# Optimization experiments

Hardware: AMD Instinct MI355X
Metric: run time of the kernel (lower is better)

The kernel has to match this reference:

```python
import jax, jax.numpy as jnp
import numpy as np

B, S, E, H = 4, 2048, 1024, 16
D = E // H  # head dim = 64


def setup_inputs() -> dict:
    key = jax.random.key(0)
    ks = jax.random.split(key, 8)
    scale = 0.02
    return {
        "query": jax.random.normal(ks[0], (B, S, E), jnp.float32),
        "keys": jax.random.normal(ks[1], (B, S, E), jnp.float32),
        "values": jax.random.normal(ks[2], (B, S, E), jnp.float32),
        "mask": jnp.ones((B, 1, 1, S), jnp.int32),
        "Wq": jax.random.normal(ks[3], (D, D), jnp.float32) * scale,
        "Wk": jax.random.normal(ks[4], (D, D), jnp.float32) * scale,
        "Wv": jax.random.normal(ks[5], (D, D), jnp.float32) * scale,
        "Wf": jax.random.normal(ks[6], (E, E), jnp.float32) * scale,
        "bf": jax.random.normal(ks[7], (E,), jnp.float32) * scale,
    }


def reference(query, keys, values, mask, Wq, Wk, Wv, Wf, bf):
    b, sq, _ = query.shape
    sk = keys.shape[1]
    # reshape to heads: [b, s, H, D]
    q = query.reshape(b, sq, H, D)
    k = keys.reshape(b, sk, H, D)
    v = values.reshape(b, sk, H, D)
    # per-head linear projections (torch Linear: x @ W.T, no bias)
    q = jnp.einsum('bshd,ed->bshe', q, Wq)
    k = jnp.einsum('bshd,ed->bshe', k, Wk)
    v = jnp.einsum('bshd,ed->bshe', v, Wv)
    # scores [b, h, q, k]
    scores = jnp.einsum('bqhd,bkhd->bhqk', q, k)
    scores = jnp.where(mask == 0, -jnp.inf, scores)
    attn = jax.nn.softmax(scores / jnp.sqrt(jnp.float32(D)), axis=3)
    # context [b, q, h, d] -> [b, q, E]
    ctx = jnp.einsum('bhqk,bkhd->bqhd', attn, v).reshape(b, sq, E)
    return ctx @ Wf.T + bf
```

## Files before the change

kernel.cpp:

```cpp
#include <hip/hip_runtime.h>

#define B_ 4
#define S_ 2048
#define E_ 1024
#define H_ 16
#define D_ 64

typedef unsigned short u16;
typedef unsigned int u32;
typedef __bf16 bf16x8 __attribute__((ext_vector_type(8)));
typedef float f32x4 __attribute__((ext_vector_type(4)));
typedef u16 u16x8 __attribute__((ext_vector_type(8)));
typedef u16 u16x4 __attribute__((ext_vector_type(4)));

#if defined(__has_builtin)
#if __has_builtin(__builtin_amdgcn_exp2f)
#define EXP2F(x) __builtin_amdgcn_exp2f(x)
#else
#define EXP2F(x) exp2f(x)
#endif
#else
#define EXP2F(x) exp2f(x)
#endif

__device__ __forceinline__ u16 bfbits(float f) {
  __bf16 h = (__bf16)f;
  return __builtin_bit_cast(u16, h);
}
__device__ __forceinline__ f32x4 mfma16(bf16x8 a, bf16x8 b, f32x4 c) {
  return __builtin_amdgcn_mfma_f32_16x16x32_bf16(a, b, c, 0, 0, 0);
}
__device__ __forceinline__ bf16x8 lds_ld8(const u16* base, int off) {
  return *reinterpret_cast<const bf16x8*>(reinterpret_cast<const char*>(base) + off);
}
__device__ __forceinline__ void gload_lds16(const u16* g, u16* l) {
  __builtin_amdgcn_global_load_lds((const __attribute__((address_space(1))) void*)g,
                                   (__attribute__((address_space(3))) void*)l, 16, 0, 0);
}

__global__ __launch_bounds__(256) void proj_kernel(
    const float* __restrict__ qin, const float* __restrict__ kin, const float* __restrict__ vin,
    const float* __restrict__ Wq, const float* __restrict__ Wk, const float* __restrict__ Wv,
    const float* __restrict__ Wf,
    u16* __restrict__ qo, u16* __restrict__ ko, u16* __restrict__ vo, u16* __restrict__ wfo)
{
  const int t = threadIdx.x;
  const int tensor = blockIdx.z >> 2, b = blockIdx.z & 3;

  if (tensor == 3) {
    int chunk = ((blockIdx.z & 3) * 16 + blockIdx.y) * 16 + blockIdx.x;
    int i = chunk * 256 + t;
    float4 f = reinterpret_cast<const float4*>(Wf)[i];
    u16x4 h4;
    h4[0] = bfbits(f.x); h4[1] = bfbits(f.y); h4[2] = bfbits(f.z); h4[3] = bfbits(f.w);
    reinterpret_cast<u16x4*>(wfo)[i] = h4;
    return;
  }

  __shared__ __align__(16) u16 Al[128 * 64];
  __shared__ __align__(16) u16 Wl[64 * 64];
  const int w = t >> 6, l = t & 63, lg = l >> 4, ln = l & 15;
  const int h = blockIdx.y, s0 = blockIdx.x * 128;

  const float* x; const float* W; float scale;
  if (tensor == 0)      { x = qin; W = Wq; scale = 0.125f * 1.44269504f; }
  else if (tensor == 1) { x = kin; W = Wk; scale = 1.0f; }
  else                  { x = vin; W = Wv; scale = 1.0f; }

  {
    const int e = t >> 2, d0 = (t & 3) * 16;
    const float4* wr = reinterpret_cast<const float4*>(W + e * 64 + d0);
    float4 f0 = wr[0], f1 = wr[1], f2 = wr[2], f3 = wr[3];
    u16x8 p0, p1;
    p0[0]=bfbits(f0.x*scale); p0[1]=bfbits(f0.y*scale); p0[2]=bfbits(f0.z*scale); p0[3]=bfbits(f0.w*scale);
    p0[4]=bfbits(f1.x*scale); p0[5]=bfbits(f1.y*scale); p0[6]=bfbits(f1.z*scale); p0[7]=bfbits(f1.w*scale);
    p1[0]=bfbits(f2.x*scale); p1[1]=bfbits(f2.y*scale); p1[2]=bfbits(f2.z*scale); p1[3]=bfbits(f2.w*scale);
    p1[4]=bfbits(f3.x*scale); p1[5]=bfbits(f3.y*scale); p1[6]=bfbits(f3.z*scale); p1[7]=bfbits(f3.w*scale);
    *reinterpret_cast<u16x8*>(reinterpret_cast<char*>(Wl) + ((e*128 + d0*2     ) ^ ((e & 7) << 4))) = p0;
    *reinterpret_cast<u16x8*>(reinterpret_cast<char*>(Wl) + ((e*128 + d0*2 + 16) ^ ((e & 7) << 4))) = p1;
  }
  {
    const int row = t >> 1, d0 = (t & 1) * 32;
    const float4* xr = reinterpret_cast<const float4*>(x + ((size_t)(b * S_ + s0 + row)) * E_ + h * D_ + d0);
    #pragma unroll
    for (int c = 0; c < 4; ++c) {
      float4 f0 = xr[2 * c], f1 = xr[2 * c + 1];
      u16x8 pk;
      pk[0]=bfbits(f0.x); pk[1]=bfbits(f0.y); pk[2]=bfbits(f0.z); pk[3]=bfbits(f0.w);
      pk[4]=bfbits(f1.x); pk[5]=bfbits(f1.y); pk[6]=bfbits(f1.z); pk[7]=bfbits(f1.w);
      *reinterpret_cast<u16x8*>(reinterpret_cast<char*>(Al) +
          ((row * 128 + (d0 + 8 * c) * 2) ^ ((row & 7) << 4))) = pk;
    }
  }
  __syncthreads();

  bf16x8 wb[4][2];
  #pragma unroll
  for (int nn = 0; nn < 4; ++nn) {
    int brow = nn * 16 + ln;
    int bo = (brow * 128 + lg * 16) ^ ((ln & 7) << 4);
    wb[nn][0] = lds_ld8(Wl, bo);
    wb[nn][1] = lds_ld8(Wl, bo ^ 64);
  }
  f32x4 acc[2][4] = {};
  #pragma unroll
  for (int sub = 0; sub < 2; ++sub) {
    int arow = 32 * w + 16 * sub + ln;
    int ao = (arow * 128 + lg * 16) ^ ((ln & 7) << 4);
    bf16x8 a0 = lds_ld8(Al, ao), a1 = lds_ld8(Al, ao ^ 64);
    #pragma unroll
    for (int nn = 0; nn < 4; ++nn) {
      acc[sub][nn] = mfma16(a0, wb[nn][0], acc[sub][nn]);
      acc[sub][nn] = mfma16(a1, wb[nn][1], acc[sub][nn]);
    }
  }

  if (tensor < 2) {
    u16* o = (tensor == 0) ? qo : ko;
    const size_t hb = ((size_t)(b * H_ + h)) * (S_ * D_);
    #pragma unroll
    for (int sub = 0; sub < 2; ++sub)
      #pragma unroll
      for (int nn = 0; nn < 4; ++nn)
        #pragma unroll
        for (int r = 0; r < 4; ++r)
          o[hb + (size_t)(s0 + 32*w + 16*sub + 4*lg + r) * D_ + nn*16 + ln] = bfbits(acc[sub][nn][r]);
  } else {
    const size_t hb = ((size_t)(b * H_ + h)) * (D_ * S_);
    #pragma unroll
    for (int sub = 0; sub < 2; ++sub)
      #pragma unroll
      for (int nn = 0; nn < 4; ++nn)
        #pragma unroll
        for (int r = 0; r < 4; ++r) {
          int scol = s0 + 32*w + 16*sub + 4*lg + r;
          int sl = scol & 63;
          int c = (sl & 3) | (((sl >> 4) & 1) << 2) | (((sl >> 2) & 3) << 3) | ((sl >> 5) << 5);
          vo[hb + (size_t)(nn*16 + ln) * S_ + (scol & ~63) + c] = bfbits(acc[sub][nn][r]);
        }
  }
}

#define QK_PHASE(SCW)                                                          \
  {                                                                            \
    __builtin_amdgcn_s_setprio(1);                                             \
    _Pragma("unroll")                                                          \
    for (int kn = 0; kn < 4; ++kn) {                                           \
      int o0 = ((ln * 128 + lg * 16) ^ ((ln & 7) << 4)) + kn * 2048;           \
      bf16x8 ka0 = lds_ld8(Kc, o0), ka1 = lds_ld8(Kc, o0 ^ 64);                \
      _Pragma("unroll")                                                        \
      for (int sub = 0; sub < 2; ++sub) {                                      \
        f32x4 z = {0.f, 0.f, 0.f, 0.f};                                        \
        z = mfma16(ka0, qb[sub][0], z);                                        \
        z = mfma16(ka1, qb[sub][1], z);                                        \
        SCW[sub][kn] = z;                                                      \
      }                                                                        \
    }                                                                          \
    __builtin_amdgcn_s_setprio(0);                                             \
  }

#define EXPPV_PHASE(SCR, KV0PREV)                                              \
  {                                                                            \
    if (!allone) {                                                             \
      const int kv0p = (KV0PREV);                                              \
      _Pragma("unroll")                                                        \
      for (int kn = 0; kn < 4; ++kn) {                                         \
        const int4 m4 = *reinterpret_cast<const int4*>(                        \
            mask + b * S_ + kv0p + kn * 16 + lg * 4);                          \
        const int* mp = reinterpret_cast<const int*>(&m4);                     \
        _Pragma("unroll")                                                      \
        for (int r = 0; r < 4; ++r)                                            \
          if (mp[r] == 0) { SCR[0][kn][r] = -1e30f; SCR[1][kn][r] = -1e30f; }  \
      }                                                                        \
    }                                                                          \
    bf16x8 pa[2][2];                                                           \
    _Pragma("unroll")                                                          \
    for (int sub = 0; sub < 2; ++sub)                                          \
      _Pragma("unroll")                                                        \
      for (int kn = 0; kn < 4; ++kn)                                           \
        _Pragma("unroll")                                                      \
        for (int r = 0; r < 4; ++r)                                            \
          pa[sub][kn >> 1][(kn & 1) * 4 + r] = (__bf16)EXP2F(SCR[sub][kn][r]); \
    __builtin_amdgcn_s_setprio(1);                                             \
    _Pragma("unroll")                                                          \
    for (int sub = 0; sub < 2; ++sub) {                                        \
      lacc[sub] = mfma16(pa[sub][0], ones, lacc[sub]);                         \
      lacc[sub] = mfma16(pa[sub][1], ones, lacc[sub]);                         \
    }                                                                          \
    _Pragma("unroll")                                                          \
    for (int kh = 0; kh < 2; ++kh)                                             \
      _Pragma("unroll")                                                        \
      for (int dn = 0; dn < 4; ++dn)                                           \
        _Pragma("unroll")                                                      \
        for (int sub = 0; sub < 2; ++sub)                                      \
          oacc[sub][dn] = mfma16(pa[sub][kh], vf[kh][dn], oacc[sub][dn]);      \
    __builtin_amdgcn_s_setprio(0);                                             \
  }

#define VREAD_PHASE                                                            \
  _Pragma("unroll")                                                            \
  for (int kh = 0; kh < 2; ++kh)                                               \
    _Pragma("unroll")                                                          \
    for (int dn = 0; dn < 4; ++dn) {                                           \
      int vo0 = ((ln * 128 + 16 * lg + 64 * kh) ^ ((ln & 7) << 4)) + dn * 2048;\
      vf[kh][dn] = lds_ld8(Vc, vo0);                                           \
    }

#define ATTN_ITER(KT, SCW, SCR, CUR, LAST)                                     \
  {                                                                            \
    const u16* Kc = &Kl[CUR][0];                                               \
    const u16* Vc = &Vl[CUR][0];                                               \
    if (!(LAST)) {                                                             \
      const int nk = ((KT) + 1) * 64;                                          \
      gload_lds16(kg + nk * D_, kd + ((CUR) ^ 1) * 4096);                      \
      gload_lds16(vg + nk,      vd + ((CUR) ^ 1) * 4096);                      \
    }                                                                          \
    QK_PHASE(SCW)                                                              \
    EXPPV_PHASE(SCR, ((KT) - 1) * 64)                                          \
    VREAD_PHASE                                                                \
    if (!(LAST)) {                                                             \
      asm volatile("s_waitcnt vmcnt(0)" ::: "memory");                         \
      __syncthreads();                                                         \
    }                                                                          \
  }

__global__ __launch_bounds__(512, 2) void attn_kernel(
    const u16* __restrict__ qw,
    const u16* __restrict__ kw,
    const u16* __restrict__ vtw,
    const int* __restrict__ mask,
    u16* __restrict__ ctx)
{
  __shared__ __align__(16) u16 Kl[2][64 * 64];
  __shared__ __align__(16) u16 Vl[2][64 * 64];
  __shared__ int s_allone;

  const int t = threadIdx.x, w = t >> 6, l = t & 63, lg = l >> 4, ln = l & 15;
  const int hb = blockIdx.x;
  const int b = hb >> 4;
  const int q0 = blockIdx.y * 256;
  const size_t koff = (size_t)hb * (S_ * D_);
  const size_t voff = (size_t)hb * (D_ * S_);

  if (t == 0) s_allone = 1;
  __syncthreads();

  const int srow = t >> 3, scol = (t & 7) ^ ((t >> 3) & 7);
  const u16* kg = kw + koff + srow * D_ + scol * 8;
  const u16* vg = vtw + voff + (size_t)srow * S_ + scol * 8;
  u16* kd = &Kl[0][0] + t * 8;
  u16* vd = &Vl[0][0] + t * 8;

  gload_lds16(kg, kd);
  gload_lds16(vg, vd);

  {
    const int4 m4 = *reinterpret_cast<const int4*>(mask + b * S_ + t * 4);
    if (!(m4.x && m4.y && m4.z && m4.w)) s_allone = 0;
  }

  bf16x8 qb[2][2];
  #pragma unroll
  for (int sub = 0; sub < 2; ++sub) {
    const u16* qp = qw + koff + (size_t)(q0 + 32*w + 16*sub + ln) * D_ + 8*lg;
    qb[sub][0] = *reinterpret_cast<const bf16x8*>(qp);
    qb[sub][1] = *reinterpret_cast<const bf16x8*>(qp + 32);
  }

  u16x8 ob;
  #pragma unroll
  for (int i = 0; i < 8; ++i) ob[i] = 0x3F80;
  const bf16x8 ones = __builtin_bit_cast(bf16x8, ob);

  f32x4 oacc[2][4] = {};
  f32x4 lacc[2] = {};
  f32x4 scA[2][4], scB[2][4];
  bf16x8 vf[2][4];

  asm volatile("s_waitcnt vmcnt(0)" ::: "memory");
  __syncthreads();
  const int allone = s_allone;

  {
    const u16* Kc = &Kl[0][0];
    const u16* Vc = &Vl[0][0];
    gload_lds16(kg + 64 * D_, kd + 4096);
    gload_lds16(vg + 64,      vd + 4096);
    QK_PHASE(scA)
    VREAD_PHASE
    asm volatile("s_waitcnt vmcnt(0)" ::: "memory");
    __syncthreads();
  }

  for (int kt = 1; kt < 31; kt += 2) {
    ATTN_ITER(kt,     scB, scA, 1, false)
    ATTN_ITER(kt + 1, scA, scB, 0, false)
  }
  ATTN_ITER(31, scB, scA, 1, true)
  EXPPV_PHASE(scB, 31 * 64)

  #pragma unroll
  for (int sub = 0; sub < 2; ++sub) {
    #pragma unroll
    for (int r = 0; r < 4; ++r) {
      float linv = 1.f / lacc[sub][r];
      int qrow = q0 + 32 * w + 16 * sub + 4 * lg + r;
      size_t base = ((size_t)b * S_ + qrow) * E_ + (hb & 15) * D_;
      #pragma unroll
      for (int dn = 0; dn < 4; ++dn)
        ctx[base + dn * 16 + ln] = bfbits(oacc[sub][dn][r] * linv);
    }
  }
}

__global__ __launch_bounds__(256, 2) void outproj_kernel(
    const u16* __restrict__ ctx, const u16* __restrict__ wf,
    const float* __restrict__ bias, float* __restrict__ out)
{
  __shared__ __align__(16) u16 Al[2][128 * 64];
  __shared__ __align__(16) u16 Bl[2][128 * 64];
  const int t = threadIdx.x, w = t >> 6, l = t & 63, lg = l >> 4, ln = l & 15;
  const int wm = w >> 1, wn = w & 1;
  const int m0 = blockIdx.x * 128, n0 = blockIdx.y * 128;
  f32x4 acc[4][4] = {};

  const u16* ag[4]; const u16* bg[4]; int ldo[4];
  #pragma unroll
  for (int it = 0; it < 4; ++it) {
    int j = it * 256 + t, row = j >> 3, c = (j & 7) ^ (row & 7);
    ag[it] = ctx + (size_t)(m0 + row) * E_ + c * 8;
    bg[it] = wf  + (size_t)(n0 + row) * E_ + c * 8;
    ldo[it] = j * 8;
  }
  #pragma unroll
  for (int it = 0; it < 4; ++it) {
    gload_lds16(ag[it], &Al[0][0] + ldo[it]);
    gload_lds16(bg[it], &Bl[0][0] + ldo[it]);
  }
  asm volatile("s_waitcnt vmcnt(0)" ::: "memory");
  __syncthreads();

  int cur = 0;
  for (int kt = 0; kt < E_ / 64; ++kt) {
    if (kt + 1 < E_ / 64) {
      const int k0 = (kt + 1) * 64;
      #pragma unroll
      for (int it = 0; it < 4; ++it) {
        gload_lds16(ag[it] + k0, &Al[cur ^ 1][0] + ldo[it]);
        gload_lds16(bg[it] + k0, &Bl[cur ^ 1][0] + ldo[it]);
      }
    }
    const u16* Ac = &Al[cur][0]; const u16* Bc = &Bl[cur][0];

    bf16x8 af[4][2], bff[4][2];
    #pragma unroll
    for (int ms = 0; ms < 4; ++ms) {
      int ar = 64 * wm + 16 * ms + ln;
      int ao = (ar * 128 + lg * 16) ^ ((ln & 7) << 4);
      af[ms][0] = lds_ld8(Ac, ao); af[ms][1] = lds_ld8(Ac, ao ^ 64);
    }
    #pragma unroll
    for (int ns = 0; ns < 4; ++ns) {
      int br = 64 * wn + 16 * ns + ln;
      int bo = (br * 128 + lg * 16) ^ ((ln & 7) << 4);
      bff[ns][0] = lds_ld8(Bc, bo); bff[ns][1] = lds_ld8(Bc, bo ^ 64);
    }
    __builtin_amdgcn_s_setprio(1);
    #pragma unroll
    for (int ms = 0; ms < 4; ++ms)
      #pragma unroll
      for (int ns = 0; ns < 4; ++ns) {
        acc[ms][ns] = mfma16(af[ms][0], bff[ns][0], acc[ms][ns]);
        acc[ms][ns] = mfma16(af[ms][1], bff[ns][1], acc[ms][ns]);
      }
    __builtin_amdgcn_s_setprio(0);

    if (kt + 1 < E_ / 64) {
      asm volatile("s_waitcnt vmcnt(0)" ::: "memory");
      __syncthreads();
      cur ^= 1;
    }
  }

  #pragma unroll
  for (int ns = 0; ns < 4; ++ns) {
    float bv = bias[n0 + 64 * wn + 16 * ns + ln];
    #pragma unroll
    for (int ms = 0; ms < 4; ++ms)
      #pragma unroll
      for (int r = 0; r < 4; ++r)
        out[(size_t)(m0 + 64*wm + 16*ms + 4*lg + r) * E_ + n0 + 64*wn + 16*ns + ln] =
            acc[ms][ns][r] + bv;
  }
}

extern "C" void kernel_launch(void* const* d_in, const int* in_sizes, int n_in,
                              void* d_out, int out_size, void* d_ws, size_t ws_size,
                              hipStream_t stream)
{
  const float* q   = (const float*)d_in[0];
  const float* k   = (const float*)d_in[1];
  const float* v   = (const float*)d_in[2];
  const int*  mask = (const int*) d_in[3];
  const float* Wq  = (const float*)d_in[4];
  const float* Wk  = (const float*)d_in[5];
  const float* Wv  = (const float*)d_in[6];
  const float* Wf  = (const float*)d_in[7];
  const float* bfv = (const float*)d_in[8];
  float* out = (float*)d_out;

  const size_t NQKV = (size_t)B_ * H_ * S_ * D_;
  const size_t NCTX = (size_t)B_ * S_ * E_;
  u16* q_ws   = (u16*)d_ws;
  u16* k_ws   = q_ws + NQKV;
  u16* v_ws   = k_ws + NQKV;
  u16* ctx_ws = v_ws + NQKV;
  u16* wf_ws  = ctx_ws + NCTX;

  proj_kernel<<<dim3(S_ / 128, H_, 16), dim3(256), 0, stream>>>(
      q, k, v, Wq, Wk, Wv, Wf, q_ws, k_ws, v_ws, wf_ws);
  attn_kernel<<<dim3(B_ * H_, S_ / 256), dim3(512), 0, stream>>>(
      q_ws, k_ws, v_ws, mask, ctx_ws);
  outproj_kernel<<<dim3((B_ * S_) / 128, E_ / 128), dim3(256), 0, stream>>>(
      ctx_ws, wf_ws, bfv, out);
}
```

Before: 127.9 us.

## Replace software-pipelined QK/PV schedule with 4-buffer two-tile-per-sync attention loop

Removes the cross-iteration software pipeline, in which the QK scores of tile k were computed alongside the exp and PV of tile k-1 and V fragments were preloaded into registers. Each tile is now computed in one pass, with V read from LDS right where it is used. LDS staging grows from two to four K/V buffers so two tiles are loaded per barrier, halving the number of syncs. Launch bounds change to request 4 blocks per CU, which raises register pressure. The loss of QK/softmax overlap and the doubled LDS footprint may hurt latency hiding and occupancy.

```diff
diff --git a/kernel.cpp b/kernel.cpp
--- a/kernel.cpp
+++ b/kernel.cpp
@@ -141,8 +141,11 @@
   }
 }
 
-#define QK_PHASE(SCW)                                                          \
+#define COMPUTE_TILE(KT, BUF)                                                  \
   {                                                                            \
+    const u16* Kc = &Kl[BUF][0];                                               \
+    const u16* Vc = &Vl[BUF][0];                                               \
+    f32x4 sc[2][4];                                                            \
     __builtin_amdgcn_s_setprio(1);                                             \
     _Pragma("unroll")                                                          \
     for (int kn = 0; kn < 4; ++kn) {                                           \
@@ -153,24 +156,20 @@
         f32x4 z = {0.f, 0.f, 0.f, 0.f};                                        \
         z = mfma16(ka0, qb[sub][0], z);                                        \
         z = mfma16(ka1, qb[sub][1], z);                                        \
-        SCW[sub][kn] = z;                                                      \
+        sc[sub][kn] = z;                                                       \
       }                                                                        \
     }                                                                          \
     __builtin_amdgcn_s_setprio(0);                                             \
-  }
-
-#define EXPPV_PHASE(SCR, KV0PREV)                                              \
-  {                                                                            \
     if (!allone) {                                                             \
-      const int kv0p = (KV0PREV);                                              \
+      const int kv0 = (KT) * 64;                                               \
       _Pragma("unroll")                                                        \
       for (int kn = 0; kn < 4; ++kn) {                                         \
         const int4 m4 = *reinterpret_cast<const int4*>(                        \
-            mask + b * S_ + kv0p + kn * 16 + lg * 4);                          \
+            mask + b * S_ + kv0 + kn * 16 + lg * 4);                           \
         const int* mp = reinterpret_cast<const int*>(&m4);                     \
         _Pragma("unroll")                                                      \
         for (int r = 0; r < 4; ++r)                                            \
-          if (mp[r] == 0) { SCR[0][kn][r] = -1e30f; SCR[1][kn][r] = -1e30f; }  \
+          if (mp[r] == 0) { sc[0][kn][r] = -1e30f; sc[1][kn][r] = -1e30f; }    \
       }                                                                        \
     }                                                                          \
     bf16x8 pa[2][2];                                                           \
@@ -180,7 +179,7 @@
       for (int kn = 0; kn < 4; ++kn)                                           \
         _Pragma("unroll")                                                      \
         for (int r = 0; r < 4; ++r)                                            \
-          pa[sub][kn >> 1][(kn & 1) * 4 + r] = (__bf16)EXP2F(SCR[sub][kn][r]); \
+          pa[sub][kn >> 1][(kn & 1) * 4 + r] = (__bf16)EXP2F(sc[sub][kn][r]);  \
     __builtin_amdgcn_s_setprio(1);                                             \
     _Pragma("unroll")                                                          \
     for (int sub = 0; sub < 2; ++sub) {                                        \
@@ -190,49 +189,25 @@
     _Pragma("unroll")                                                          \
     for (int kh = 0; kh < 2; ++kh)                                             \
       _Pragma("unroll")                                                        \
-      for (int dn = 0; dn < 4; ++dn)                                           \
+      for (int dn = 0; dn < 4; ++dn) {                                         \
+        int vo0 = ((ln * 128 + 16 * lg + 64 * kh) ^ ((ln & 7) << 4)) + dn * 2048; \
+        bf16x8 vb = lds_ld8(Vc, vo0);                                          \
         _Pragma("unroll")                                                      \
         for (int sub = 0; sub < 2; ++sub)                                      \
-          oacc[sub][dn] = mfma16(pa[sub][kh], vf[kh][dn], oacc[sub][dn]);      \
+          oacc[sub][dn] = mfma16(pa[sub][kh], vb, oacc[sub][dn]);              \
+      }                                                                        \
     __builtin_amdgcn_s_setprio(0);                                             \
   }
 
-#define VREAD_PHASE                                                            \
-  _Pragma("unroll")                                                            \
-  for (int kh = 0; kh < 2; ++kh)                                               \
-    _Pragma("unroll")                                                          \
-    for (int dn = 0; dn < 4; ++dn) {                                           \
-      int vo0 = ((ln * 128 + 16 * lg + 64 * kh) ^ ((ln & 7) << 4)) + dn * 2048;\
-      vf[kh][dn] = lds_ld8(Vc, vo0);                                           \
-    }
-
-#define ATTN_ITER(KT, SCW, SCR, CUR, LAST)                                     \
-  {                                                                            \
-    const u16* Kc = &Kl[CUR][0];                                               \
-    const u16* Vc = &Vl[CUR][0];                                               \
-    if (!(LAST)) {                                                             \
-      const int nk = ((KT) + 1) * 64;                                          \
-      gload_lds16(kg + nk * D_, kd + ((CUR) ^ 1) * 4096);                      \
-      gload_lds16(vg + nk,      vd + ((CUR) ^ 1) * 4096);                      \
-    }                                                                          \
-    QK_PHASE(SCW)                                                              \
-    EXPPV_PHASE(SCR, ((KT) - 1) * 64)                                          \
-    VREAD_PHASE                                                                \
-    if (!(LAST)) {                                                             \
-      asm volatile("s_waitcnt vmcnt(0)" ::: "memory");                         \
-      __syncthreads();                                                         \
-    }                                                                          \
-  }
-
-__global__ __launch_bounds__(512, 2) void attn_kernel(
+__global__ __launch_bounds__(512, 4) void attn_kernel(
     const u16* __restrict__ qw,
     const u16* __restrict__ kw,
     const u16* __restrict__ vtw,
     const int* __restrict__ mask,
     u16* __restrict__ ctx)
 {
-  __shared__ __align__(16) u16 Kl[2][64 * 64];
-  __shared__ __align__(16) u16 Vl[2][64 * 64];
+  __shared__ __align__(16) u16 Kl[4][64 * 64];
+  __shared__ __align__(16) u16 Vl[4][64 * 64];
   __shared__ int s_allone;
 
   const int t = threadIdx.x, w = t >> 6, l = t & 63, lg = l >> 4, ln = l & 15;
@@ -248,11 +223,14 @@
   const int srow = t >> 3, scol = (t & 7) ^ ((t >> 3) & 7);
   const u16* kg = kw + koff + srow * D_ + scol * 8;
   const u16* vg = vtw + voff + (size_t)srow * S_ + scol * 8;
-  u16* kd = &Kl[0][0] + t * 8;
-  u16* vd = &Vl[0][0] + t * 8;
-
-  gload_lds16(kg, kd);
-  gload_lds16(vg, vd);
+  u16* kd[4]; u16* vd[4];
+  #pragma unroll
+  for (int i = 0; i < 4; ++i) { kd[i] = &Kl[i][0] + t * 8; vd[i] = &Vl[i][0] + t * 8; }
+
+  gload_lds16(kg, kd[0]);
+  gload_lds16(vg, vd[0]);
+  gload_lds16(kg + 64 * D_, kd[1]);
+  gload_lds16(vg + 64,      vd[1]);
 
   {
     const int4 m4 = *reinterpret_cast<const int4*>(mask + b * S_ + t * 4);
@@ -274,30 +252,39 @@
 
   f32x4 oacc[2][4] = {};
   f32x4 lacc[2] = {};
-  f32x4 scA[2][4], scB[2][4];
-  bf16x8 vf[2][4];
 
   asm volatile("s_waitcnt vmcnt(0)" ::: "memory");
   __syncthreads();
   const int allone = s_allone;
 
-  {
-    const u16* Kc = &Kl[0][0];
-    const u16* Vc = &Vl[0][0];
-    gload_lds16(kg + 64 * D_, kd + 4096);
-    gload_lds16(vg + 64,      vd + 4096);
-    QK_PHASE(scA)
-    VREAD_PHASE
-    asm volatile("s_waitcnt vmcnt(0)" ::: "memory");
-    __syncthreads();
-  }
-
-  for (int kt = 1; kt < 31; kt += 2) {
-    ATTN_ITER(kt,     scB, scA, 1, false)
-    ATTN_ITER(kt + 1, scA, scB, 0, false)
-  }
-  ATTN_ITER(31, scB, scA, 1, true)
-  EXPPV_PHASE(scB, 31 * 64)
+  for (int kt = 0; kt < 32; kt += 4) {
+    if (kt + 2 < 32) {
+      gload_lds16(kg + (kt + 2) * 64 * D_, kd[2]);
+      gload_lds16(vg + (kt + 2) * 64,      vd[2]);
+      gload_lds16(kg + (kt + 3) * 64 * D_, kd[3]);
+      gload_lds16(vg + (kt + 3) * 64,      vd[3]);
+    }
+    COMPUTE_TILE(kt,     0)
+    COMPUTE_TILE(kt + 1, 1)
+    if (kt + 2 < 32) {
+      asm volatile("s_waitcnt vmcnt(0)" ::: "memory");
+      __syncthreads();
+    }
+    if (kt + 4 < 32) {
+      gload_lds16(kg + (kt + 4) * 64 * D_, kd[0]);
+      gload_lds16(vg + (kt + 4) * 64,      vd[0]);
+      gload_lds16(kg + (kt + 5) * 64 * D_, kd[1]);
+      gload_lds16(vg + (kt + 5) * 64,      vd[1]);
+    }
+    if (kt + 2 < 32) {
+      COMPUTE_TILE(kt + 2, 2)
+      COMPUTE_TILE(kt + 3, 3)
+    }
+    if (kt + 4 < 32) {
+      asm volatile("s_waitcnt vmcnt(0)" ::: "memory");
+      __syncthreads();
+    }
+  }
 
   #pragma unroll
   for (int sub = 0; sub < 2; ++sub) {
```

Result: faster. 117.4 us (-8.2%).
